# Performance work log

Hardware: AMD Instinct MI355X
Metric: run time of the kernel (lower is better)

## Reference

```python
import jax, jax.numpy as jnp
import numpy as np

B = 16; SEQ_LEN = 96; PRED_LEN = 96; N_VARS = 862; D_MODEL = 512; D_FF = 1024
N_HEADS = 8; E_LAYERS = 2; D_FREQ = 512; KF_LEN = 5000; ALPHA = 0.5; TOP_P = 0.5
FREQ_DIM = SEQ_LEN // 2 + 1            # rfft bins = 49
KEY_LEN = int(np.ceil(FREQ_DIM * ALPHA))  # 25 -> y_freq in_features = 50
KERNEL = 25; NOISE_EPS = 0.01; LN_EPS = 1e-5; REVIN_EPS = 1e-5


def setup_inputs() -> dict:
    ks = iter(jax.random.split(jax.random.key(0), 64))
    def g(*shape):
        return jax.random.normal(next(ks), shape, jnp.float32) * 0.02
    z = lambda *s: jnp.zeros(s, jnp.float32)
    o = lambda *s: jnp.ones(s, jnp.float32)
    inp = {}
    inp['x_enc'] = jax.random.normal(next(ks), (B, SEQ_LEN, N_VARS), jnp.float32)
    inp['gate_noise'] = jax.random.normal(next(ks), (N_VARS,), jnp.float32)
    inp['revin_w'] = o(N_VARS); inp['revin_b'] = z(N_VARS)
    inp['fc2_w'] = g(SEQ_LEN, D_MODEL); inp['fc2_b'] = z(D_MODEL)
    inp['fc3_w'] = g(D_MODEL, PRED_LEN); inp['fc3_b'] = z(PRED_LEN)
    inp['fc4_w'] = g(SEQ_LEN, D_MODEL); inp['fc4_b'] = z(D_MODEL)
    inp['fc5_w'] = g(D_MODEL, PRED_LEN); inp['fc5_b'] = z(PRED_LEN)
    inp['tc_w1'] = g(D_MODEL, D_MODEL // 2); inp['tc_w2'] = g(D_MODEL // 2, N_VARS)
    inp['tn_w1'] = g(D_MODEL, D_MODEL // 2); inp['tn_w2'] = g(D_MODEL // 2, N_VARS)
    inp['lt_w1'] = g(SEQ_LEN, D_MODEL); inp['lt_b1'] = z(D_MODEL)
    inp['lt_w2'] = g(D_MODEL, D_MODEL); inp['lt_b2'] = z(D_MODEL)
    inp['yf_w'] = g(2 * KEY_LEN, D_FREQ); inp['yf_b'] = z(D_FREQ)
    inp['ls_w1'] = g(D_FREQ, D_FREQ); inp['ls_b1'] = z(D_FREQ)
    inp['ls_w2'] = g(D_FREQ, D_FREQ); inp['ls_b2'] = z(D_FREQ)
    inp['fco_w'] = g(2 * D_MODEL, PRED_LEN); inp['fco_b'] = z(PRED_LEN)
    inp['freq_table'] = jax.random.normal(next(ks), (KF_LEN, N_VARS), jnp.float32)
    inp['enc_wq'] = g(E_LAYERS, D_MODEL, D_MODEL); inp['enc_bq'] = z(E_LAYERS, D_MODEL)
    inp['enc_wk'] = g(E_LAYERS, D_MODEL, D_MODEL); inp['enc_bk'] = z(E_LAYERS, D_MODEL)
    inp['enc_wv'] = g(E_LAYERS, D_MODEL, D_MODEL); inp['enc_bv'] = z(E_LAYERS, D_MODEL)
    inp['enc_wo'] = g(E_LAYERS, D_MODEL, D_MODEL); inp['enc_bo'] = z(E_LAYERS, D_MODEL)
    inp['enc_c1w'] = g(E_LAYERS, D_MODEL, D_FF); inp['enc_c1b'] = z(E_LAYERS, D_FF)
    inp['enc_c2w'] = g(E_LAYERS, D_FF, D_MODEL); inp['enc_c2b'] = z(E_LAYERS, D_MODEL)
    inp['enc_g1'] = o(E_LAYERS, D_MODEL); inp['enc_be1'] = z(E_LAYERS, D_MODEL)
    inp['enc_g2'] = o(E_LAYERS, D_MODEL); inp['enc_be2'] = z(E_LAYERS, D_MODEL)
    inp['norm_g'] = o(D_MODEL); inp['norm_b'] = z(D_MODEL)
    inp['batch_key_frequency'] = jax.random.randint(next(ks), (B,), 0, KF_LEN)
    return inp


def _lrelu(t):
    return jnp.where(t >= 0, t, 0.01 * t)


def _layernorm(x, g, b):
    m = jnp.mean(x, -1, keepdims=True)
    v = jnp.mean((x - m) ** 2, -1, keepdims=True)
    return (x - m) * jax.lax.rsqrt(v + LN_EPS) * g + b


def _decomp(x):
    # moving_avg(kernel=25, stride=1) with edge replication padding, via cumsum
    pad = (KERNEL - 1) // 2
    xp = jnp.concatenate([jnp.repeat(x[:, :1], pad, axis=1), x,
                          jnp.repeat(x[:, -1:], pad, axis=1)], axis=1)
    c = jnp.cumsum(xp, axis=1)
    c = jnp.concatenate([jnp.zeros_like(c[:, :1]), c], axis=1)
    mean = (c[:, KERNEL:] - c[:, :-KERNEL]) / KERNEL  # [B, L, N]
    return x - mean, mean


def _kf_gather(table, index, length):
    # data[(index[:,None] + arange(length)) % KF_LEN] -> [B, length, N]
    gi = (index[:, None] + jnp.arange(length)[None, :]) % KF_LEN
    return table[gi]


def _forward(x_enc, gate_noise, revin_w, revin_b, fc2_w, fc2_b, fc3_w, fc3_b,
             fc4_w, fc4_b, fc5_w, fc5_b, tc_w1, tc_w2, tn_w1, tn_w2,
             lt_w1, lt_b1, lt_w2, lt_b2, yf_w, yf_b, ls_w1, ls_b1, ls_w2, ls_b2,
             fco_w, fco_b, freq_table, enc_wq, enc_bq, enc_wk, enc_bk, enc_wv, enc_bv,
             enc_wo, enc_bo, enc_c1w, enc_c1b, enc_c2w, enc_c2b,
             enc_g1, enc_be1, enc_g2, enc_be2, norm_g, norm_b, batch_key_frequency):
    # RevIN norm (stats detached, as in RevIN)
    mean = jax.lax.stop_gradient(jnp.mean(x_enc, axis=1, keepdims=True))
    std = jax.lax.stop_gradient(jnp.sqrt(jnp.var(x_enc, axis=1, keepdims=True) + REVIN_EPS))
    x = (x_enc - mean) / std * revin_w + revin_b  # [B, L, N]

    # ---- Frequency encoder ----
    _, trend = _decomp(x)
    t = _lrelu(trend.transpose(0, 2, 1) @ lt_w1 + lt_b1) @ lt_w2 + lt_b2  # [B,N,D]
    xf = jnp.fft.rfft(x.transpose(0, 2, 1), axis=-1, norm='ortho')  # [B,N,FREQ_DIM]
    y_key = jnp.concatenate([xf.real[..., :KEY_LEN], xf.imag[..., :KEY_LEN]], axis=-1)
    y_key = y_key @ yf_w + yf_b  # [B,N,D_FREQ]
    y_key = y_key.transpose(0, 2, 1) - _kf_gather(freq_table, batch_key_frequency, D_FREQ)
    y = _lrelu(y_key.transpose(0, 2, 1) @ ls_w1 + ls_b1) @ ls_w2 + ls_b2  # [B,N,D_FREQ]
    y = y.transpose(0, 2, 1) + _kf_gather(freq_table, (batch_key_frequency + D_FREQ) % KF_LEN, D_FREQ)
    y = y.transpose(0, 2, 1)  # [B,N,D_FREQ], real part of frequency coeffs
    x_fre = jnp.fft.irfft(y.astype(jnp.complex64), n=SEQ_LEN, axis=-1, norm='ortho')  # [B,N,L]
    x_fre = x_fre @ fc4_w + fc4_b + t  # [B,N,D]
    x_fre_loss = x_fre @ fc5_w + fc5_b  # [B,N,pred]

    # ---- Time encoder ----
    xb = x.transpose(0, 2, 1) @ fc2_w + fc2_b  # [B,N,D]
    # noisy top-p gating mask
    xc = jax.nn.relu(xb @ tc_w1) @ tc_w2
    xn = jax.nn.relu(xb @ tn_w1) @ tn_w2
    # nn.Softplus(beta=-1): -log(1+exp(-x)) = -softplus(-x)
    xe = xc + gate_noise * (-jax.nn.softplus(-(xn + NOISE_EPS)))
    xmin = jnp.min(xe, axis=-1, keepdims=True)
    xmax = jnp.max(xe, axis=-1, keepdims=True)
    logits = (xe - xmin) / (xmax - xmin + 1e-6) + jnp.eye(N_VARS, dtype=xe.dtype)
    mask = (logits < TOP_P)[:, None]  # [B,1,N,N], True = masked out

    scale = 1.0 / np.sqrt(D_MODEL // N_HEADS)
    for l in range(E_LAYERS):
        q = (xb @ enc_wq[l] + enc_bq[l]).reshape(B, N_VARS, N_HEADS, -1)
        k = (xb @ enc_wk[l] + enc_bk[l]).reshape(B, N_VARS, N_HEADS, -1)
        v = (xb @ enc_wv[l] + enc_bv[l]).reshape(B, N_VARS, N_HEADS, -1)
        s = jnp.einsum('blhe,bshe->bhls', q, k)
        s = jnp.where(mask, -jnp.inf, s)
        a = jax.nn.softmax(scale * s, axis=-1)
        o = jnp.einsum('bhls,bshd->blhd', a, v).reshape(B, N_VARS, D_MODEL)
        xb = xb + (o @ enc_wo[l] + enc_bo[l])
        xb = _layernorm(xb, enc_g1[l], enc_be1[l])
        yff = jax.nn.gelu(xb @ enc_c1w[l] + enc_c1b[l], approximate=False) @ enc_c2w[l] + enc_c2b[l]
        xb = _layernorm(xb + yff, enc_g2[l], enc_be2[l])
    xb = _layernorm(xb, norm_g, norm_b)
    x_time_loss = xb @ fc3_w + fc3_b  # [B,N,pred]

    dec = (jnp.concatenate([xb, x_fre], axis=-1) @ fco_w + fco_b).transpose(0, 2, 1)  # [B,pred,N]

    def _denorm(z):
        return ((z - revin_b) / (revin_w + REVIN_EPS * REVIN_EPS)) * std + mean

    dec = _denorm(dec)
    x_time_loss = _denorm(x_time_loss.transpose(0, 2, 1))
    x_fre_loss = _denorm(x_fre_loss.transpose(0, 2, 1))
    return dec[:, -PRED_LEN:, :], x_time_loss, x_fre_loss


def reference(x_enc, gate_noise, revin_w, revin_b, fc2_w, fc2_b, fc3_w, fc3_b,
              fc4_w, fc4_b, fc5_w, fc5_b, tc_w1, tc_w2, tn_w1, tn_w2,
              lt_w1, lt_b1, lt_w2, lt_b2, yf_w, yf_b, ls_w1, ls_b1, ls_w2, ls_b2,
              fco_w, fco_b, freq_table, enc_wq, enc_bq, enc_wk, enc_bk, enc_wv, enc_bv,
              enc_wo, enc_bo, enc_c1w, enc_c1b, enc_c2w, enc_c2b,
              enc_g1, enc_be1, enc_g2, enc_be2, norm_g, norm_b, batch_key_frequency):
    return _forward(x_enc, gate_noise, revin_w, revin_b, fc2_w, fc2_b, fc3_w, fc3_b,
                    fc4_w, fc4_b, fc5_w, fc5_b, tc_w1, tc_w2, tn_w1, tn_w2,
                    lt_w1, lt_b1, lt_w2, lt_b2, yf_w, yf_b, ls_w1, ls_b1, ls_w2, ls_b2,
                    fco_w, fco_b, freq_table, enc_wq, enc_bq, enc_wk, enc_bk, enc_wv, enc_bv,
                    enc_wo, enc_bo, enc_c1w, enc_c1b, enc_c2w, enc_c2b,
                    enc_g1, enc_be1, enc_g2, enc_be2, norm_g, norm_b, batch_key_frequency)
```

## Files before the change

kernel.cpp:

```cpp
#include <hip/hip_runtime.h>
#include <hip/hip_bf16.h>
#include <math.h>

typedef __hip_bfloat16 bf16;
typedef unsigned long long u64;
using s8v = __attribute__((ext_vector_type(8))) short;
using f4v = __attribute__((ext_vector_type(4))) float;

#define B_   16
#define L_   96
#define NV   862
#define DM   512
#define NH   8
#define DH   64
#define KFL  5000
#define NBN  (B_*NV)
#define NVP  896
#define QKVW 1536
#define L2P  128

#define BAR()  __builtin_amdgcn_s_barrier()
#define SCB()  __builtin_amdgcn_sched_barrier(0)
#define VMW0() asm volatile("s_waitcnt vmcnt(0)" ::: "memory")
#define VMW4() asm volatile("s_waitcnt vmcnt(4)" ::: "memory")
#define VMW6() asm volatile("s_waitcnt vmcnt(6)" ::: "memory")
#define VMW8() asm volatile("s_waitcnt vmcnt(8)" ::: "memory")

__device__ __forceinline__ float tof(bf16 x)  { return __bfloat162float(x); }

__device__ __forceinline__ int sxl(int r, int c) {
    return (r << 6) + ((c ^ (r & 7)) << 3);
}
__device__ __forceinline__ int px(int r, int k) {
    return (r << 6) + (((((k >> 3) ^ (r & 7)) + ((r & 8) >> 2)) & 7) << 3) + (k & 7);
}
__device__ __forceinline__ int pxc(int r, int c) {
    return (r << 6) + ((((c ^ (r & 7)) + ((r & 8) >> 2)) & 7) << 3);
}

__device__ __forceinline__ void gl16(const bf16* g, bf16* l)
{
    __builtin_amdgcn_global_load_lds(
        (const __attribute__((address_space(1))) void*)g,
        (__attribute__((address_space(3))) void*)l, 16, 0, 0);
}

__device__ __forceinline__ void stage64(const bf16* __restrict__ src, int ld,
                                        int r0, int rmax, int k0, bf16* buf, int tid)
{
    #pragma unroll
    for (int i = 0; i < 2; i++) {
        int e = tid + i * 256;
        int r = e >> 3, c = e & 7;
        int gr = r0 + r; gr = gr > rmax ? rmax : gr;
        int gk = k0 + ((c ^ (r & 7)) << 3);
        gl16(src + (size_t)gr * ld + gk, buf + ((size_t)(e >> 6) << 9));
    }
}
__device__ __forceinline__ void stage128(const bf16* __restrict__ src, int ld,
                                         int r0, int rmax, int k0, bf16* buf, int tid)
{
    #pragma unroll
    for (int i = 0; i < 4; i++) {
        int e = tid + i * 256;
        int r = e >> 3, c = e & 7;
        int gr = r0 + r; gr = gr > rmax ? rmax : gr;
        int gk = k0 + ((c ^ (r & 7)) << 3);
        gl16(src + (size_t)gr * ld + gk, buf + ((size_t)(e >> 6) << 9));
    }
}

__device__ __forceinline__ int xcd_swz(int orig, int nwg)
{
    int q = nwg >> 3, r = nwg & 7;
    int xc = orig & 7, loc = orig >> 3;
    return (xc < r ? xc * (q + 1) : r * (q + 1) + (xc - r) * q) + loc;
}

__global__ void detect_k(const unsigned short* __restrict__ rw, int* __restrict__ flag)
{
    if (threadIdx.x == 0 && blockIdx.x == 0)
        *flag = (rw[0] == 0 && rw[2] == 0 && rw[4] == 0) ? 1 : 0;
}

struct CB { const void* src[30]; bf16* dst[30]; int n[30]; int so[30]; };
__global__ __launch_bounds__(256)
void cvtb_k(CB cb, const int* __restrict__ flag)
{
    int t = blockIdx.y;
    int i = blockIdx.x * 256 + threadIdx.x;
    if (i >= cb.n[t]) return;
    int s = cb.so[t] + i;
    if (*flag) cb.dst[t][i] = __float2bfloat16(((const float*)cb.src[t])[s]);
    else       cb.dst[t][i] = ((const bf16*)cb.src[t])[s];
}

#define NWT 24
struct WD { const void* src; bf16* dst; int K, Kp, N; long srcOff; };
struct WTB { WD d[NWT]; };
__global__ __launch_bounds__(256)
void wtcb_k(WTB wb, const int* __restrict__ flag)
{
    __shared__ bf16 tile[32][33];
    WD dd = wb.d[blockIdx.z];
    int n0 = blockIdx.x * 32, k0 = blockIdx.y * 32;
    if (n0 >= dd.N || k0 >= dd.Kp) return;
    int tx = threadIdx.x & 31, ty = threadIdx.x >> 5;
    int f32 = *flag;
    #pragma unroll
    for (int r = 0; r < 4; r++) {
        int k = k0 + ty + r * 8, n = n0 + tx;
        bf16 v = __float2bfloat16(0.f);
        if (k < dd.K && n < dd.N)
            v = f32 ? __float2bfloat16(((const float*)dd.src)[dd.srcOff + (size_t)k * dd.N + n])
                    : ((const bf16*)dd.src)[dd.srcOff + (size_t)k * dd.N + n];
        tile[ty + r * 8][tx] = v;
    }
    __syncthreads();
    #pragma unroll
    for (int r = 0; r < 4; r++) {
        int n = n0 + ty + r * 8, k = k0 + tx;
        if (n < dd.N && k < dd.Kp) dd.dst[(size_t)n * dd.Kp + k] = tile[tx][ty + r * 8];
    }
}

__global__ __launch_bounds__(256)
void vt_k(const bf16* __restrict__ qkv, bf16* __restrict__ Vt)
{
    __shared__ bf16 t[32][33];
    int bh = blockIdx.z;
    int n0 = blockIdx.x * 32, d0 = blockIdx.y * 32;
    int b = bh >> 3, h = bh & 7;
    int tx = threadIdx.x & 31, ty = threadIdx.x >> 5;
    #pragma unroll
    for (int r = 0; r < 4; r++) {
        int n = n0 + ty + r * 8, d = d0 + tx;
        bf16 v = __float2bfloat16(0.f);
        if (n < NV) v = qkv[(size_t)(b * NV + n) * QKVW + 1024 + h * DH + d];
        t[ty + r * 8][tx] = v;
    }
    __syncthreads();
    #pragma unroll
    for (int r = 0; r < 4; r++) {
        int d = d0 + ty + r * 8, n = n0 + tx;
        Vt[((size_t)bh * DH + d) * NVP + n] = t[tx][ty + r * 8];
    }
}

__global__ __launch_bounds__(128)
void revin_k(const void* __restrict__ x_enc, const bf16* __restrict__ rw,
             const bf16* __restrict__ rb, bf16* __restrict__ xT,
             bf16* __restrict__ trend, float* __restrict__ meanA,
             float* __restrict__ stdA, const int* __restrict__ flag)
{
    int row = blockIdx.x;
    int b = row / NV, n = row - b * NV;
    int tid = threadIdx.x;
    int f32 = *flag;
    __shared__ float xr[96];
    __shared__ float part[2][2];
    __shared__ float mv[2];
    float v = 0.f;
    if (tid < 96) {
        size_t idx = ((size_t)b * L_ + tid) * NV + n;
        v = f32 ? ((const float*)x_enc)[idx] : tof(((const bf16*)x_enc)[idx]);
    }
    float s = v, sq = v * v;
    #pragma unroll
    for (int off = 32; off; off >>= 1) {
        s  += __shfl_xor(s,  off, 64);
        sq += __shfl_xor(sq, off, 64);
    }
    int wid = tid >> 6;
    if ((tid & 63) == 0) { part[wid][0] = s; part[wid][1] = sq; }
    __syncthreads();
    if (tid == 0) {
        float S = part[0][0] + part[1][0], Q = part[0][1] + part[1][1];
        float m = S / 96.f;
        float var = fmaxf(Q / 96.f - m * m, 0.f);
        float st = sqrtf(var + 1e-5f);
        mv[0] = m; mv[1] = st;
        meanA[row] = m; stdA[row] = st;
    }
    __syncthreads();
    float m = mv[0], st = mv[1];
    const bf16 z16 = __float2bfloat16(0.f);
    if (tid < 96) {
        float xv = (v - m) / st * tof(rw[n]) + tof(rb[n]);
        xr[tid] = xv;
        xT[(size_t)row * L2P + tid] = __float2bfloat16(xv);
    } else {
        xT[(size_t)row * L2P + tid] = z16;
    }
    __syncthreads();
    if (tid < 96) {
        float acc = 0.f;
        #pragma unroll
        for (int d = -12; d <= 12; d++) {
            int k = tid + d;
            k = k < 0 ? 0 : (k > 95 ? 95 : k);
            acc += xr[k];
        }
        trend[(size_t)row * L2P + tid] = __float2bfloat16(acc * (1.f / 25.f));
    } else {
        trend[(size_t)row * L2P + tid] = z16;
    }
}

__global__ void myf_k(const bf16* __restrict__ yf_w, bf16* __restrict__ MyfT)
{
    int idx = blockIdx.x * 256 + threadIdx.x;
    if (idx >= 512 * L2P) return;
    int d = idx >> 7, l = idx & 127;
    const float invs = 0.10206207261596575f;
    float acc = 0.f;
    if (l < 96) {
        for (int f = 0; f < 25; f++) {
            float ang = (float)(f * l) / 48.0f;
            acc += cospif(ang) * tof(yf_w[f * 512 + d]);
            acc -= sinpif(ang) * tof(yf_w[(25 + f) * 512 + d]);
        }
        acc *= invs;
    }
    MyfT[(size_t)d * L2P + l] = __float2bfloat16(acc);
}

__global__ void ceff_k(const bf16* __restrict__ fc4_w, bf16* __restrict__ CeffT)
{
    int idx = blockIdx.x * 256 + threadIdx.x;
    if (idx >= 512 * 64) return;
    int d = idx >> 6, f = idx & 63;
    const float invs = 0.10206207261596575f;
    float acc = 0.f;
    if (f < 49) {
        for (int l = 0; l < 96; l++) {
            float coef;
            if (f == 0)       coef = 1.f;
            else if (f == 48) coef = (l & 1) ? -1.f : 1.f;
            else              coef = 2.f * cospif((float)(f * l) / 48.f);
            acc += coef * tof(fc4_w[l * 512 + d]);
        }
        acc *= invs;
    }
    CeffT[(size_t)d * 64 + f] = __float2bfloat16(acc);
}

__device__ __forceinline__ float epi(float v, int n, int m, int N, int act,
                                     const bf16* bias, const float* Res,
                                     const void* ft, const int* kf,
                                     const int* dflag)
{
    if (act >= 5) {
        v += tof(bias[n]);
        int b = m / NV, nv = m - b * NV;
        int gi = (act == 5) ? (kf[b] + n) % KFL : (kf[b] + 512 + n) % KFL;
        size_t gidx = (size_t)gi * NV + nv;
        float fv = (*dflag) ? ((const float*)ft)[gidx] : tof(((const bf16*)ft)[gidx]);
        return (act == 5) ? v - fv : v + fv;
    }
    if (act == 4) {
        float z = -(v + 0.01f);
        float sp = fmaxf(z, 0.f) + log1pf(expf(-fabsf(z)));
        return Res[(size_t)m * N + n] + tof(bias[n]) * (-sp);
    }
    if (bias) v += tof(bias[n]);
    if (Res)  v += Res[(size_t)m * N + n];
    if (act == 1)      v = fmaxf(v, 0.f);
    else if (act == 2) v = (v >= 0.f) ? v : 0.01f * v;
    else if (act == 3) v = 0.5f * v * (1.f + erff(v * 0.70710678118654752f));
    return v;
}

__global__ __launch_bounds__(256)
void gemm128c(const bf16* __restrict__ A, int lda,
              const bf16* __restrict__ Wt, int ldb,
              const bf16* __restrict__ bias, const float* Res,
              float* C32, bf16* C16, int M, int N, int K, int act, int gx)
{
    __shared__ __align__(16) bf16 As[2][128 * 64];
    __shared__ __align__(16) bf16 Bs[2][128 * 64];
    int tid = threadIdx.x;
    int w = tid >> 6, lane = tid & 63;
    int lr = lane >> 4, lc = lane & 15;
    int nid = xcd_swz(blockIdx.x, gridDim.x);
    int bx = nid % gx, by = nid / gx;
    int row0 = by * 128, col0 = bx * 128;
    int mq = (w >> 1) * 64, nq = (w & 1) * 64;
    f4v acc[4][4] = {};
    int nt = K >> 6;
    stage128(A, lda, row0, M - 1, 0, As[0], tid);
    stage128(Wt, ldb, col0, N - 1, 0, Bs[0], tid);
    if (nt > 1) {
        stage128(A, lda, row0, M - 1, 64, As[1], tid);
        stage128(Wt, ldb, col0, N - 1, 64, Bs[1], tid);
        VMW8();
    } else {
        VMW0();
    }
    BAR(); SCB();
    for (int t = 0; t < nt; t++) {
        int cur = t & 1;
        #pragma unroll
        for (int sub = 0; sub < 2; sub++) {
            int ck = sub * 4 + lr;
            s8v a[4], b[4];
            #pragma unroll
            for (int mt = 0; mt < 4; mt++) a[mt] = *(const s8v*)&As[cur][sxl(mq + mt * 16 + lc, ck)];
            #pragma unroll
            for (int j = 0; j < 4; j++) b[j] = *(const s8v*)&Bs[cur][sxl(nq + j * 16 + lc, ck)];
            #pragma unroll
            for (int mt = 0; mt < 4; mt++)
                #pragma unroll
                for (int j = 0; j < 4; j++)
                    acc[mt][j] = __builtin_amdgcn_mfma_f32_16x16x32_bf16(a[mt], b[j], acc[mt][j], 0, 0, 0);
        }
        if (t + 1 < nt) {
            SCB(); BAR(); SCB();
            if (t + 2 < nt) {
                stage128(A, lda, row0, M - 1, (t + 2) << 6, As[cur], tid);
                stage128(Wt, ldb, col0, N - 1, (t + 2) << 6, Bs[cur], tid);
                VMW8();
            } else {
                VMW0();
            }
            BAR(); SCB();
        }
    }
    #pragma unroll
    for (int mt = 0; mt < 4; mt++)
    #pragma unroll
    for (int j = 0; j < 4; j++) {
        #pragma unroll
        for (int r = 0; r < 4; r++) {
            int m = row0 + mq + mt * 16 + lr * 4 + r;
            int n = col0 + nq + j * 16 + lc;
            if (m >= M || n >= N) continue;
            float v = epi(acc[mt][j][r], n, m, N, act, bias, Res, nullptr, nullptr, nullptr);
            if (C32) C32[(size_t)m * N + n] = v;
            if (C16) C16[(size_t)m * N + n] = __float2bfloat16(v);
        }
    }
}

__global__ __launch_bounds__(256)
void gemm64c(const bf16* __restrict__ A, int lda,
             const bf16* __restrict__ Wt, int ldb,
             const bf16* __restrict__ bias, const float* Res,
             float* C32, bf16* C16, int M, int N, int K, int act,
             const void* ft, const int* kf, const int* dflag, int gx)
{
    __shared__ __align__(16) bf16 As[2][64 * 64];
    __shared__ __align__(16) bf16 Bs[2][128 * 64];
    int tid = threadIdx.x;
    int w = tid >> 6, lane = tid & 63;
    int lr = lane >> 4, lc = lane & 15;
    int nid = xcd_swz(blockIdx.x, gridDim.x);
    int bx = nid % gx, by = nid / gx;
    int row0 = by * 64, col0 = bx * 128;
    int mq = (w >> 1) * 32, nq = (w & 1) * 64;
    f4v acc[2][4] = {};
    int nt = K >> 6;
    stage64(A, lda, row0, M - 1, 0, As[0], tid);
    stage128(Wt, ldb, col0, N - 1, 0, Bs[0], tid);
    if (nt > 1) {
        stage64(A, lda, row0, M - 1, 64, As[1], tid);
        stage128(Wt, ldb, col0, N - 1, 64, Bs[1], tid);
        VMW6();
    } else {
        VMW0();
    }
    BAR(); SCB();
    for (int t = 0; t < nt; t++) {
        int cur = t & 1;
        #pragma unroll
        for (int sub = 0; sub < 2; sub++) {
            int ck = sub * 4 + lr;
            s8v a[2], b[4];
            #pragma unroll
            for (int mt = 0; mt < 2; mt++) a[mt] = *(const s8v*)&As[cur][sxl(mq + mt * 16 + lc, ck)];
            #pragma unroll
            for (int j = 0; j < 4; j++) b[j] = *(const s8v*)&Bs[cur][sxl(nq + j * 16 + lc, ck)];
            #pragma unroll
            for (int mt = 0; mt < 2; mt++)
                #pragma unroll
                for (int j = 0; j < 4; j++)
                    acc[mt][j] = __builtin_amdgcn_mfma_f32_16x16x32_bf16(a[mt], b[j], acc[mt][j], 0, 0, 0);
        }
        if (t + 1 < nt) {
            SCB(); BAR(); SCB();
            if (t + 2 < nt) {
                stage64(A, lda, row0, M - 1, (t + 2) << 6, As[cur], tid);
                stage128(Wt, ldb, col0, N - 1, (t + 2) << 6, Bs[cur], tid);
                VMW6();
            } else {
                VMW0();
            }
            BAR(); SCB();
        }
    }
    #pragma unroll
    for (int mt = 0; mt < 2; mt++)
    #pragma unroll
    for (int j = 0; j < 4; j++) {
        #pragma unroll
        for (int r = 0; r < 4; r++) {
            int m = row0 + mq + mt * 16 + lr * 4 + r;
            int n = col0 + nq + j * 16 + lc;
            if (m >= M || n >= N) continue;
            float v = epi(acc[mt][j][r], n, m, N, act, bias, Res, ft, kf, dflag);
            if (C32) C32[(size_t)m * N + n] = v;
            if (C16) C16[(size_t)m * N + n] = __float2bfloat16(v);
        }
    }
}

__global__ __launch_bounds__(256)
void outg_mfma(const bf16* __restrict__ xb16, const bf16* __restrict__ xfre16,
               const bf16* __restrict__ fcoT, const bf16* __restrict__ fc3T,
               const bf16* __restrict__ fc5T, const bf16* __restrict__ fcob,
               const bf16* __restrict__ fc3b, const bf16* __restrict__ fc5b,
               const bf16* __restrict__ rw, const bf16* __restrict__ rb,
               const float* __restrict__ meanA, const float* __restrict__ stdA,
               void* __restrict__ outv, const int* __restrict__ flag)
{
    __shared__ __align__(16) bf16 As[2][64 * 64];
    __shared__ __align__(16) bf16 Bs[2][64 * 64];
    const int M = NBN, N = 96;
    const size_t OSZ = (size_t)B_ * L_ * NV;
    int z = blockIdx.z;
    const bf16 *A1, *W1, *A2 = nullptr, *W2 = nullptr, *bias;
    int ldb; size_t obase;
    if (z == 0) { A1 = xb16; W1 = fcoT; A2 = xfre16; W2 = fcoT + 512; ldb = 1024; bias = fcob; obase = 0; }
    else if (z == 1) { A1 = xb16; W1 = fc3T; ldb = 512; bias = fc3b; obase = OSZ; }
    else { A1 = xfre16; W1 = fc5T; ldb = 512; bias = fc5b; obase = 2 * OSZ; }
    int tid = threadIdx.x;
    int w = tid >> 6, lane = tid & 63;
    int lr = lane >> 4, lc = lane & 15;
    int row0 = blockIdx.y * 64, col0 = blockIdx.x * 64;
    int mq = (w >> 1) * 32, nq = (w & 1) * 32;
    int f32o = *flag;
    f4v acc[2][2] = {};
    int nt = (z == 0) ? 16 : 8;
    stage64(A1, 512, row0, M - 1, 0, As[0], tid);
    stage64(W1, ldb, col0, N - 1, 0, Bs[0], tid);
    stage64(A1, 512, row0, M - 1, 64, As[1], tid);
    stage64(W1, ldb, col0, N - 1, 64, Bs[1], tid);
    VMW4();
    BAR(); SCB();
    for (int t = 0; t < nt; t++) {
        int cur = t & 1;
        #pragma unroll
        for (int sub = 0; sub < 2; sub++) {
            int ck = sub * 4 + lr;
            s8v a0 = *(const s8v*)&As[cur][sxl(mq + lc, ck)];
            s8v a1 = *(const s8v*)&As[cur][sxl(mq + 16 + lc, ck)];
            s8v b0 = *(const s8v*)&Bs[cur][sxl(nq + lc, ck)];
            s8v b1 = *(const s8v*)&Bs[cur][sxl(nq + 16 + lc, ck)];
            acc[0][0] = __builtin_amdgcn_mfma_f32_16x16x32_bf16(a0, b0, acc[0][0], 0, 0, 0);
            acc[0][1] = __builtin_amdgcn_mfma_f32_16x16x32_bf16(a0, b1, acc[0][1], 0, 0, 0);
            acc[1][0] = __builtin_amdgcn_mfma_f32_16x16x32_bf16(a1, b0, acc[1][0], 0, 0, 0);
            acc[1][1] = __builtin_amdgcn_mfma_f32_16x16x32_bf16(a1, b1, acc[1][1], 0, 0, 0);
        }
        if (t + 1 < nt) {
            SCB(); BAR(); SCB();
            if (t + 2 < nt) {
                int tn = t + 2;
                const bf16* Ax = (z == 0 && tn >= 8) ? A2 : A1;
                const bf16* Wx = (z == 0 && tn >= 8) ? W2 : W1;
                stage64(Ax, 512, row0, M - 1, (tn & 7) << 6, As[cur], tid);
                stage64(Wx, ldb, col0, N - 1, (tn & 7) << 6, Bs[cur], tid);
                VMW4();
            } else {
                VMW0();
            }
            BAR(); SCB();
        }
    }
    #pragma unroll
    for (int mt = 0; mt < 2; mt++)
    #pragma unroll
    for (int j = 0; j < 2; j++) {
        #pragma unroll
        for (int r = 0; r < 4; r++) {
            int m = row0 + mq + mt * 16 + lr * 4 + r;
            int c = col0 + nq + j * 16 + lc;
            if (m >= M || c >= N) continue;
            int b = m / NV, n = m - b * NV;
            float v = acc[mt][j][r] + tof(bias[c]);
            v = (v - tof(rb[n])) / (tof(rw[n]) + 1e-10f) * stdA[m] + meanA[m];
            size_t oidx = obase + ((size_t)b * L_ + c) * NV + n;
            if (f32o) ((float*)outv)[oidx] = v;
            else      ((bf16*)outv)[oidx] = __float2bfloat16(v);
        }
    }
}

__global__ __launch_bounds__(256)
void gating_k(const float* __restrict__ xe, u64* __restrict__ mask64)
{
    int row = blockIdx.x;
    int i = row % NV;
    int tid = threadIdx.x;
    size_t base = (size_t)row * NV;
    float vals[4];
    int cnt = 0;
    float mn = INFINITY, mx = -INFINITY;
    for (int j = tid; j < NV; j += 256) {
        float e = xe[base + j];
        vals[cnt++] = e;
        mn = fminf(mn, e);
        mx = fmaxf(mx, e);
    }
    #pragma unroll
    for (int off = 32; off; off >>= 1) {
        mn = fminf(mn, __shfl_xor(mn, off, 64));
        mx = fmaxf(mx, __shfl_xor(mx, off, 64));
    }
    __shared__ float smn[4], smx[4], fin[2];
    int w = tid >> 6, lane = tid & 63;
    if (lane == 0) { smn[w] = mn; smx[w] = mx; }
    __syncthreads();
    if (tid == 0) {
        float a = fminf(fminf(smn[0], smn[1]), fminf(smn[2], smn[3]));
        float c = fmaxf(fmaxf(smx[0], smx[1]), fmaxf(smx[2], smx[3]));
        fin[0] = a;
        fin[1] = 1.f / (c - a + 1e-6f);
    }
    __syncthreads();
    float a = fin[0], inv = fin[1];
    cnt = 0;
    for (int t = w; t < 14; t += 4) {
        int j = t * 64 + lane;
        bool masked = true;
        if (j < NV) {
            float lg = (vals[cnt++] - a) * inv + ((j == i) ? 1.f : 0.f);
            masked = (lg < 0.5f);
        }
        u64 word = __ballot(masked);
        if (lane == 0) mask64[(size_t)row * 16 + t] = word;
    }
}

__global__ __launch_bounds__(256)
void ln_k(const float* __restrict__ X, const bf16* __restrict__ g,
          const bf16* __restrict__ bta, float* __restrict__ Y32,
          bf16* __restrict__ Y16)
{
    int row = blockIdx.x;
    int tid = threadIdx.x;
    size_t base = (size_t)row * DM;
    float v0 = X[base + tid], v1 = X[base + tid + 256];
    float s = v0 + v1, sq = v0 * v0 + v1 * v1;
    #pragma unroll
    for (int off = 32; off; off >>= 1) {
        s  += __shfl_xor(s,  off, 64);
        sq += __shfl_xor(sq, off, 64);
    }
    __shared__ float ps[4], pq[4], mv[2];
    int wid = tid >> 6;
    if ((tid & 63) == 0) { ps[wid] = s; pq[wid] = sq; }
    __syncthreads();
    if (tid == 0) {
        float S = ps[0] + ps[1] + ps[2] + ps[3];
        float Q = pq[0] + pq[1] + pq[2] + pq[3];
        float m = S / 512.f;
        float var = fmaxf(Q / 512.f - m * m, 0.f);
        mv[0] = m;
        mv[1] = rsqrtf(var + 1e-5f);
    }
    __syncthreads();
    float m = mv[0], r = mv[1];
    float o0 = (v0 - m) * r * tof(g[tid])       + tof(bta[tid]);
    float o1 = (v1 - m) * r * tof(g[tid + 256]) + tof(bta[tid + 256]);
    if (Y32) { Y32[base + tid] = o0; Y32[base + tid + 256] = o1; }
    if (Y16) { Y16[base + tid] = __float2bfloat16(o0);
               Y16[base + tid + 256] = __float2bfloat16(o1); }
}

__global__ __launch_bounds__(256)
void ln2x_k(const float* __restrict__ X, const bf16* __restrict__ g1,
            const bf16* __restrict__ b1, const bf16* __restrict__ g2,
            const bf16* __restrict__ b2, bf16* __restrict__ Y16)
{
    int row = blockIdx.x;
    int tid = threadIdx.x;
    size_t base = (size_t)row * DM;
    float v0 = X[base + tid], v1 = X[base + tid + 256];
    __shared__ float ps[4], pq[4], mv[2];
    int wid = tid >> 6;
    {
        float s = v0 + v1, sq = v0 * v0 + v1 * v1;
        #pragma unroll
        for (int off = 32; off; off >>= 1) {
            s  += __shfl_xor(s,  off, 64);
            sq += __shfl_xor(sq, off, 64);
        }
        if ((tid & 63) == 0) { ps[wid] = s; pq[wid] = sq; }
        __syncthreads();
        if (tid == 0) {
            float S = ps[0] + ps[1] + ps[2] + ps[3];
            float Q = pq[0] + pq[1] + pq[2] + pq[3];
            float m = S / 512.f;
            float var = fmaxf(Q / 512.f - m * m, 0.f);
            mv[0] = m; mv[1] = rsqrtf(var + 1e-5f);
        }
        __syncthreads();
    }
    float m1 = mv[0], r1 = mv[1];
    float y0 = (v0 - m1) * r1 * tof(g1[tid])       + tof(b1[tid]);
    float y1 = (v1 - m1) * r1 * tof(g1[tid + 256]) + tof(b1[tid + 256]);
    __syncthreads();
    {
        float s = y0 + y1, sq = y0 * y0 + y1 * y1;
        #pragma unroll
        for (int off = 32; off; off >>= 1) {
            s  += __shfl_xor(s,  off, 64);
            sq += __shfl_xor(sq, off, 64);
        }
        if ((tid & 63) == 0) { ps[wid] = s; pq[wid] = sq; }
        __syncthreads();
        if (tid == 0) {
            float S = ps[0] + ps[1] + ps[2] + ps[3];
            float Q = pq[0] + pq[1] + pq[2] + pq[3];
            float m = S / 512.f;
            float var = fmaxf(Q / 512.f - m * m, 0.f);
            mv[0] = m; mv[1] = rsqrtf(var + 1e-5f);
        }
        __syncthreads();
    }
    float m2 = mv[0], r2 = mv[1];
    Y16[base + tid]       = __float2bfloat16((y0 - m2) * r2 * tof(g2[tid])       + tof(b2[tid]));
    Y16[base + tid + 256] = __float2bfloat16((y1 - m2) * r2 * tof(g2[tid + 256]) + tof(b2[tid + 256]));
}

__global__ __launch_bounds__(256)
void attn_k(const bf16* __restrict__ qkv, const bf16* __restrict__ Vt,
            const u64* __restrict__ mask64, bf16* __restrict__ O)
{
    int bid = blockIdx.x;
    int bh = bid & 127;
    int q0 = (bid >> 7) * 64;
    int b = bh >> 3, h = bh & 7;
    int tid = threadIdx.x;
    int w = tid >> 6, lane = tid & 63;
    int lr = lane >> 4, lc = lane & 15;
    __shared__ bf16 Pt[4][16 * 64];
    size_t hb = (size_t)h * DH;
    int qw = q0 + w * 16;
    const float C = 0.18033688011112042f;

    s8v qf[2];
    #pragma unroll
    for (int sub = 0; sub < 2; sub++) {
        int gq = qw + lc;
        uint4 v = make_uint4(0, 0, 0, 0);
        if (gq < NV)
            v = *(const uint4*)(qkv + ((size_t)(b * NV + gq)) * QKVW + hb + sub * 32 + lr * 8);
        qf[sub] = *(s8v*)&v;
    }

    const bf16* kbase = qkv + (size_t)b * NV * QKVW + 512 + hb;
    const bf16* vbase = Vt + (size_t)bh * DH * NVP;

    float lsum[4] = {0.f, 0.f, 0.f, 0.f};
    f4v oacc[4] = {};

    for (int t = 0; t < 14; t++) {
        int j0 = t * 64;
        s8v kf[4][2];
        #pragma unroll
        for (int nt = 0; nt < 4; nt++) {
            int key = j0 + nt * 16 + lc;
            const bf16* kp = kbase + (size_t)(key < NV ? key : 0) * QKVW + lr * 8;
            kf[nt][0] = *(const s8v*)(kp);
            kf[nt][1] = *(const s8v*)(kp + 32);
        }
        f4v s[4];
        __builtin_amdgcn_s_setprio(1);
        #pragma unroll
        for (int nt = 0; nt < 4; nt++) {
            f4v sacc = {0.f, 0.f, 0.f, 0.f};
            sacc = __builtin_amdgcn_mfma_f32_16x16x32_bf16(qf[0], kf[nt][0], sacc, 0, 0, 0);
            sacc = __builtin_amdgcn_mfma_f32_16x16x32_bf16(qf[1], kf[nt][1], sacc, 0, 0, 0);
            s[nt] = sacc;
        }
        __builtin_amdgcn_s_setprio(0);
        #pragma unroll
        for (int r = 0; r < 4; r++) {
            int gq = qw + lr * 4 + r;
            u64 wd = (gq < NV) ? mask64[(size_t)(b * NV + gq) * 16 + t] : ~0ull;
            #pragma unroll
            for (int nt = 0; nt < 4; nt++) {
                float p = ((wd >> (nt * 16 + lc)) & 1) ? 0.f : exp2f(s[nt][r] * C);
                Pt[w][px(lr * 4 + r, nt * 16 + lc)] = __float2bfloat16(p);
                lsum[r] += p;
            }
        }
        s8v vv[2][4];
        #pragma unroll
        for (int sub = 0; sub < 2; sub++)
            #pragma unroll
            for (int dt = 0; dt < 4; dt++)
                vv[sub][dt] = *(const s8v*)(vbase + (size_t)(dt * 16 + lc) * NVP
                                            + j0 + (sub * 4 + lr) * 8);
        #pragma unroll
        for (int sub = 0; sub < 2; sub++) {
            s8v pa = *(const s8v*)&Pt[w][pxc(lc, sub * 4 + lr)];
            __builtin_amdgcn_s_setprio(1);
            #pragma unroll
            for (int dt = 0; dt < 4; dt++)
                oacc[dt] = __builtin_amdgcn_mfma_f32_16x16x32_bf16(pa, vv[sub][dt], oacc[dt], 0, 0, 0);
            __builtin_amdgcn_s_setprio(0);
        }
    }
    #pragma unroll
    for (int r = 0; r < 4; r++) {
        #pragma unroll
        for (int o2 = 1; o2 < 16; o2 <<= 1) lsum[r] += __shfl_xor(lsum[r], o2, 64);
    }
    #pragma unroll
    for (int r = 0; r < 4; r++) {
        int gq = qw + lr * 4 + r;
        if (gq >= NV) continue;
        float linv = 1.f / fmaxf(lsum[r], 1e-30f);
        #pragma unroll
        for (int dt = 0; dt < 4; dt++)
            O[((size_t)(b * NV + gq)) * DM + hb + dt * 16 + lc] =
                __float2bfloat16(oacc[dt][r] * linv);
    }
}

static void G1(hipStream_t s, const bf16* A, int lda, const bf16* Wt, int ldb,
               const bf16* bias, const float* Res, float* C32, bf16* C16,
               int M, int N, int K, int act)
{
    int gx = (N + 127) / 128, gy = (M + 127) / 128;
    gemm128c<<<dim3(gx * gy), 256, 0, s>>>(A, lda, Wt, ldb, bias, Res, C32, C16, M, N, K, act, gx);
}
static void G64(hipStream_t s, const bf16* A, int lda, const bf16* Wt, int ldb,
                const bf16* bias, const float* Res, float* C32, bf16* C16,
                int M, int N, int K, int act,
                const void* ft = nullptr, const int* kf = nullptr, const int* df = nullptr)
{
    int gx = (N + 127) / 128, gy = (M + 63) / 64;
    gemm64c<<<dim3(gx * gy), 256, 0, s>>>(A, lda, Wt, ldb, bias, Res, C32, C16, M, N, K, act, ft, kf, df, gx);
}

enum { I_XENC = 0, I_GNOISE, I_RW, I_RB, I_FC2W, I_FC2B, I_FC3W, I_FC3B,
       I_FC4W, I_FC4B, I_FC5W, I_FC5B, I_TCW1, I_TCW2, I_TNW1, I_TNW2,
       I_LTW1, I_LTB1, I_LTW2, I_LTB2, I_YFW, I_YFB, I_LSW1, I_LSB1,
       I_LSW2, I_LSB2, I_FCOW, I_FCOB, I_FT, I_EWQ, I_EBQ, I_EWK, I_EBK,
       I_EWV, I_EBV, I_EWO, I_EBO, I_C1W, I_C1B, I_C2W, I_C2B,
       I_G1, I_BE1, I_G2, I_BE2, I_NG, I_NB };

extern "C" void kernel_launch(void* const* d_in, const int* in_sizes, int n_in,
                              void* d_out, int out_size, void* d_ws, size_t ws_size,
                              hipStream_t stream)
{
    const int* bkey = (const int*)d_in[47];
    (void)ws_size; (void)in_sizes; (void)n_in; (void)out_size;

    float* ws = (float*)d_ws;
    size_t off = 0;
    auto alloc = [&](size_t nf) { nf = (nf + 3) & ~(size_t)3; float* p = ws + off; off += nf; return p; };
    auto balloc = [&](size_t nb) { return (bf16*)alloc((nb + 1) / 2); };
    int*  flag  = (int*)alloc(16);
    bf16* gnoise = balloc(862); bf16* rw = balloc(862); bf16* rb = balloc(862);
    bf16* fc2b = balloc(512);  bf16* fc3b = balloc(96);
    bf16* fc4w_c = balloc(49152); bf16* fc4b = balloc(512); bf16* fc5b = balloc(96);
    bf16* ltb1 = balloc(512);  bf16* ltb2 = balloc(512);
    bf16* yfw_c = balloc(25600); bf16* yfb = balloc(512);
    bf16* lsb1 = balloc(512);  bf16* lsb2 = balloc(512);
    bf16* fcob = balloc(96);
    bf16* qkvb = balloc(2 * QKVW);
    bf16* ebo = balloc(1024);  bf16* c1b = balloc(2048); bf16* c2b = balloc(1024);
    bf16* g1v = balloc(1024);  bf16* be1v = balloc(1024);
    bf16* g2v = balloc(1024);  bf16* be2v = balloc(1024);
    bf16* ngv = balloc(512);   bf16* nbv = balloc(512);
    bf16* fc2wT = balloc(512 * L2P);  bf16* fc3wT = balloc(49152); bf16* fc5wT = balloc(49152);
    bf16* lt1T = balloc(512 * L2P);   bf16* lt2T = balloc(262144);
    bf16* ls1T = balloc(262144);  bf16* ls2T = balloc(262144);
    bf16* fcoT = balloc(98304);
    bf16* tc2T = balloc(220672);  bf16* tn2T = balloc(220672);
    bf16* gate1w = balloc(262144);
    bf16* qkvw = balloc(2 * QKVW * 512);
    bf16* woT = balloc(524288);
    bf16* c1T = balloc(1048576);  bf16* c2T = balloc(1048576);
    bf16* xT    = balloc((size_t)NBN * L2P);
    bf16* trend = balloc((size_t)NBN * L2P);
    float* meanA = alloc(13824);
    float* stdA  = alloc(13824);
    bf16* MyfT  = balloc(512 * L2P);
    bf16* CeffT = balloc(512 * 64);
    bf16* y49   = balloc((size_t)NBN * 64);
    float* xb32 = alloc((size_t)NBN * 512);
    bf16* xb16  = balloc((size_t)NBN * 512);
    bf16* xfre16 = balloc((size_t)NBN * 512);
    bf16* tmp16 = balloc((size_t)NBN * 1024);
    float* fbuf = alloc((size_t)NBN * 512);
    float* gbuf = alloc((size_t)NBN * 1024);
    u64* mask64 = (u64*)alloc((size_t)NBN * 32);

    float* xe = gbuf;
    bf16* yA  = (bf16*)gbuf;
    bf16* qkv16 = (bf16*)gbuf;
    bf16* O16 = qkv16 + (size_t)NBN * QKVW;
    bf16* Vt  = tmp16;

    detect_k<<<1, 64, 0, stream>>>((const unsigned short*)d_in[I_RW], flag);

    {
        CB cb;
        int k = 0;
        auto add = [&](int idx, bf16* dst, int n, int so) {
            cb.src[k] = d_in[idx]; cb.dst[k] = dst; cb.n[k] = n; cb.so[k] = so; k++;
        };
        add(I_GNOISE, gnoise, 862, 0); add(I_RW, rw, 862, 0); add(I_RB, rb, 862, 0);
        add(I_FC2B, fc2b, 512, 0); add(I_FC3B, fc3b, 96, 0);
        add(I_FC4W, fc4w_c, 49152, 0); add(I_FC4B, fc4b, 512, 0); add(I_FC5B, fc5b, 96, 0);
        add(I_LTB1, ltb1, 512, 0); add(I_LTB2, ltb2, 512, 0);
        add(I_YFW, yfw_c, 25600, 0); add(I_YFB, yfb, 512, 0);
        add(I_LSB1, lsb1, 512, 0); add(I_LSB2, lsb2, 512, 0);
        add(I_FCOB, fcob, 96, 0);
        add(I_EBQ, qkvb + 0, 512, 0);          add(I_EBQ, qkvb + QKVW, 512, 512);
        add(I_EBK, qkvb + 512, 512, 0);        add(I_EBK, qkvb + QKVW + 512, 512, 512);
        add(I_EBV, qkvb + 1024, 512, 0);       add(I_EBV, qkvb + QKVW + 1024, 512, 512);
        add(I_EBO, ebo, 1024, 0); add(I_C1B, c1b, 2048, 0); add(I_C2B, c2b, 1024, 0);
        add(I_G1, g1v, 1024, 0); add(I_BE1, be1v, 1024, 0);
        add(I_G2, g2v, 1024, 0); add(I_BE2, be2v, 1024, 0);
        add(I_NG, ngv, 512, 0); add(I_NB, nbv, 512, 0);
        cvtb_k<<<dim3(192, 30), 256, 0, stream>>>(cb, flag);
    }

    {
        WTB wb;
        int k = 0;
        auto add = [&](int idx, bf16* dst, int K, int Kp, int N, long soff) {
            wb.d[k].src = d_in[idx]; wb.d[k].dst = dst;
            wb.d[k].K = K; wb.d[k].Kp = Kp; wb.d[k].N = N; wb.d[k].srcOff = soff; k++;
        };
        add(I_FC2W, fc2wT, 96, L2P, 512, 0);
        add(I_FC3W, fc3wT, 512, 512, 96, 0);
        add(I_FC5W, fc5wT, 512, 512, 96, 0);
        add(I_LTW1, lt1T, 96, L2P, 512, 0);
        add(I_LTW2, lt2T, 512, 512, 512, 0);
        add(I_LSW1, ls1T, 512, 512, 512, 0);
        add(I_LSW2, ls2T, 512, 512, 512, 0);
        add(I_FCOW, fcoT, 1024, 1024, 96, 0);
        add(I_TCW2, tc2T, 256, 256, 862, 0);
        add(I_TNW2, tn2T, 256, 256, 862, 0);
        add(I_TCW1, gate1w, 512, 512, 256, 0);
        add(I_TNW1, gate1w + 256 * 512, 512, 512, 256, 0);
        for (int l = 0; l < 2; l++) {
            add(I_EWO, woT + (size_t)l * 262144, 512, 512, 512, (long)l * 262144);
            add(I_C1W, c1T + (size_t)l * 524288, 512, 512, 1024, (long)l * 524288);
            add(I_C2W, c2T + (size_t)l * 524288, 1024, 1024, 512, (long)l * 524288);
            add(I_EWQ, qkvw + (size_t)l * 786432 + 0,      512, 512, 512, (long)l * 262144);
            add(I_EWK, qkvw + (size_t)l * 786432 + 262144, 512, 512, 512, (long)l * 262144);
            add(I_EWV, qkvw + (size_t)l * 786432 + 524288, 512, 512, 512, (long)l * 262144);
        }
        wtcb_k<<<dim3(32, 32, NWT), 256, 0, stream>>>(wb, flag);
    }

    revin_k<<<NBN, 128, 0, stream>>>(d_in[I_XENC], rw, rb, xT, trend, meanA, stdA, flag);
    myf_k<<<(512 * L2P + 255) / 256, 256, 0, stream>>>(yfw_c, MyfT);
    ceff_k<<<(512 * 64 + 255) / 256, 256, 0, stream>>>(fc4w_c, CeffT);

    G64(stream, trend, L2P, lt1T, L2P, ltb1, nullptr, nullptr, tmp16, NBN, 512, L2P, 2);
    G64(stream, tmp16, 512, lt2T, 512, ltb2, nullptr, fbuf, nullptr, NBN, 512, 512, 0);
    G64(stream, xT, L2P, MyfT, L2P, yfb, nullptr, nullptr, yA, NBN, 512, L2P, 5,
        d_in[I_FT], bkey, flag);
    G64(stream, yA, 512, ls1T, 512, lsb1, nullptr, nullptr, tmp16, NBN, 512, 512, 2);
    G64(stream, tmp16, 512, ls2T, 512, lsb2, nullptr, nullptr, y49, NBN, 64, 512, 6,
        d_in[I_FT], bkey, flag);
    G64(stream, y49, 64, CeffT, 64, fc4b, fbuf, nullptr, xfre16, NBN, 512, 64, 0);

    G64(stream, xT, L2P, fc2wT, L2P, fc2b, nullptr, xb32, xb16, NBN, 512, L2P, 0);

    G64(stream, xb16, 512, gate1w, 512, nullptr, nullptr, nullptr, tmp16, NBN, 512, 512, 1);
    G64(stream, tmp16, 512, tc2T, 256, nullptr, nullptr, xe, nullptr, NBN, 862, 256, 0);
    G64(stream, tmp16 + 256, 512, tn2T, 256, gnoise, xe, xe, nullptr, NBN, 862, 256, 4);
    gating_k<<<NBN, 256, 0, stream>>>(xe, mask64);

    for (int l = 0; l < 2; l++) {
        G1(stream, xb16, 512, qkvw + (size_t)l * QKVW * 512, 512,
           qkvb + l * QKVW, nullptr, nullptr, qkv16, NBN, QKVW, 512, 0);
        vt_k<<<dim3(NVP / 32, DH / 32, B_ * NH), 256, 0, stream>>>(qkv16, Vt);
        attn_k<<<dim3(14 * 128), 256, 0, stream>>>(qkv16, Vt, mask64, O16);
        G64(stream, O16, 512, woT + (size_t)l * 262144, 512, ebo + l * 512,
            xb32, fbuf, nullptr, NBN, 512, 512, 0);
        ln_k<<<NBN, 256, 0, stream>>>(fbuf, g1v + l * 512, be1v + l * 512, xb32, xb16);
        G1(stream, xb16, 512, c1T + (size_t)l * 524288, 512, c1b + l * 1024,
           nullptr, nullptr, tmp16, NBN, 1024, 512, 3);
        G64(stream, tmp16, 1024, c2T + (size_t)l * 524288, 1024, c2b + l * 512,
            xb32, fbuf, nullptr, NBN, 512, 1024, 0);
        if (l == 0)
            ln_k<<<NBN, 256, 0, stream>>>(fbuf, g2v, be2v, xb32, xb16);
        else
            ln2x_k<<<NBN, 256, 0, stream>>>(fbuf, g2v + 512, be2v + 512, ngv, nbv, xb16);
    }

    outg_mfma<<<dim3(2, (NBN + 63) / 64, 3), 256, 0, stream>>>(
        xb16, xfre16, fcoT, fc3wT, fc5wT, fcob, fc3b, fc5b,
        rw, rb, meanA, stdA, d_out, flag);
}
```

Baseline: 1.764 ms.

## Stage attention K and V tiles through double-buffered LDS with prefetch

```diff
diff --git a/kernel.cpp b/kernel.cpp
--- a/kernel.cpp
+++ b/kernel.cpp
@@ -637,6 +637,9 @@
 void attn_k(const bf16* __restrict__ qkv, const bf16* __restrict__ Vt,
             const u64* __restrict__ mask64, bf16* __restrict__ O)
 {
+    __shared__ __align__(16) bf16 Ks[2][64 * 64];
+    __shared__ __align__(16) bf16 Vs[2][64 * 64];
+    __shared__ bf16 Pt[4][16 * 64];
     int bid = blockIdx.x;
     int bh = bid & 127;
     int q0 = (bid >> 7) * 64;
@@ -644,7 +647,6 @@
     int tid = threadIdx.x;
     int w = tid >> 6, lane = tid & 63;
     int lr = lane >> 4, lc = lane & 15;
-    __shared__ bf16 Pt[4][16 * 64];
     size_t hb = (size_t)h * DH;
     int qw = q0 + w * 16;
     const float C = 0.18033688011112042f;
@@ -664,24 +666,27 @@
 
     float lsum[4] = {0.f, 0.f, 0.f, 0.f};
     f4v oacc[4] = {};
-
-    for (int t = 0; t < 14; t++) {
-        int j0 = t * 64;
-        s8v kf[4][2];
-        #pragma unroll
-        for (int nt = 0; nt < 4; nt++) {
-            int key = j0 + nt * 16 + lc;
-            const bf16* kp = kbase + (size_t)(key < NV ? key : 0) * QKVW + lr * 8;
-            kf[nt][0] = *(const s8v*)(kp);
-            kf[nt][1] = *(const s8v*)(kp + 32);
-        }
+    const int NT = 14;
+
+    stage64(kbase, QKVW, 0, NV - 1, 0, Ks[0], tid);
+    stage64(vbase, NVP, 0, DH - 1, 0, Vs[0], tid);
+    stage64(kbase, QKVW, 64, NV - 1, 0, Ks[1], tid);
+    stage64(vbase, NVP, 0, DH - 1, 64, Vs[1], tid);
+    VMW4();
+    BAR(); SCB();
+
+    for (int t = 0; t < NT; t++) {
+        int cur = t & 1;
         f4v s[4];
         __builtin_amdgcn_s_setprio(1);
         #pragma unroll
         for (int nt = 0; nt < 4; nt++) {
             f4v sacc = {0.f, 0.f, 0.f, 0.f};
-            sacc = __builtin_amdgcn_mfma_f32_16x16x32_bf16(qf[0], kf[nt][0], sacc, 0, 0, 0);
-            sacc = __builtin_amdgcn_mfma_f32_16x16x32_bf16(qf[1], kf[nt][1], sacc, 0, 0, 0);
+            #pragma unroll
+            for (int sub = 0; sub < 2; sub++) {
+                s8v bb = *(const s8v*)&Ks[cur][sxl(nt * 16 + lc, sub * 4 + lr)];
+                sacc = __builtin_amdgcn_mfma_f32_16x16x32_bf16(qf[sub], bb, sacc, 0, 0, 0);
+            }
             s[nt] = sacc;
         }
         __builtin_amdgcn_s_setprio(0);
@@ -696,21 +701,28 @@
                 lsum[r] += p;
             }
         }
-        s8v vv[2][4];
-        #pragma unroll
-        for (int sub = 0; sub < 2; sub++)
-            #pragma unroll
-            for (int dt = 0; dt < 4; dt++)
-                vv[sub][dt] = *(const s8v*)(vbase + (size_t)(dt * 16 + lc) * NVP
-                                            + j0 + (sub * 4 + lr) * 8);
         #pragma unroll
         for (int sub = 0; sub < 2; sub++) {
             s8v pa = *(const s8v*)&Pt[w][pxc(lc, sub * 4 + lr)];
             __builtin_amdgcn_s_setprio(1);
             #pragma unroll
-            for (int dt = 0; dt < 4; dt++)
-                oacc[dt] = __builtin_amdgcn_mfma_f32_16x16x32_bf16(pa, vv[sub][dt], oacc[dt], 0, 0, 0);
+            for (int dt = 0; dt < 4; dt++) {
+                s8v vv = *(const s8v*)&Vs[cur][sxl(dt * 16 + lc, sub * 4 + lr)];
+                oacc[dt] = __builtin_amdgcn_mfma_f32_16x16x32_bf16(pa, vv, oacc[dt], 0, 0, 0);
+            }
             __builtin_amdgcn_s_setprio(0);
+        }
+        if (t + 1 < NT) {
+            SCB(); BAR(); SCB();
+            if (t + 2 < NT) {
+                int j2 = (t + 2) * 64;
+                stage64(kbase, QKVW, j2, NV - 1, 0, Ks[cur], tid);
+                stage64(vbase, NVP, 0, DH - 1, j2, Vs[cur], tid);
+                VMW4();
+            } else {
+                VMW0();
+            }
+            BAR(); SCB();
         }
     }
     #pragma unroll
```

After: 1.563 ms. 1.13x faster.
